# Performance work log

Measured on AMD Instinct MI355X. Metric: run time of the kernel, lower is better.

Reference implementation:

```python
import jax, jax.numpy as jnp
import numpy as np

N_HEAD = 8


def _axial_attn(x, wq, wk, wv, fw, fb, axis):
    # x: (B, T, H, W, C); axis is the axial axis in (B, nh, T, H, W, d): 2=T, 3=H, 4=W
    B, T, H, W, C = x.shape
    d = C // N_HEAD

    def heads(y):
        # (B,T,H,W,C) -> (B, nh, T, H, W, d)
        return jnp.moveaxis(y.reshape(B, T, H, W, N_HEAD, d), -2, 1)

    q, k, v = heads(x @ wq), heads(x @ wk), heads(x @ wv)
    # restrict attention to the axial axis: move it to -2, all other dims are batch
    q = jnp.moveaxis(q, axis, -2)
    k = jnp.moveaxis(k, axis, -2)
    v = jnp.moveaxis(v, axis, -2)
    scale = 1.0 / jnp.sqrt(jnp.asarray(d, x.dtype))
    scores = jnp.einsum('...ld,...md->...lm', q * scale, k)
    att = jax.nn.softmax(scores, axis=-1)
    o = jnp.einsum('...lm,...md->...ld', att, v)
    o = jnp.moveaxis(o, -2, axis)            # restore axial axis position
    o = jnp.moveaxis(o, 1, -2).reshape(B, T, H, W, C)  # merge heads
    return o @ fw + fb


def setup_inputs() -> dict:
    key = jax.random.key(0)
    ks = jax.random.split(key, 16)
    C = 512
    x = jax.random.normal(ks[0], (4, C, 16, 32, 32), jnp.float32)
    s = 0.02

    def w(k):
        return jax.random.normal(k, (C, C), jnp.float32) * s

    inp = {'x': x}
    i = 1
    for ax in ('w', 'h', 't'):
        inp[f'wq_{ax}'] = w(ks[i])
        inp[f'wk_{ax}'] = w(ks[i + 1])
        inp[f'wv_{ax}'] = w(ks[i + 2])
        inp[f'fc_{ax}'] = w(ks[i + 3])
        inp[f'fb_{ax}'] = jnp.zeros((C,), jnp.float32)
        i += 4
    return inp


def reference(x, wq_w, wk_w, wv_w, fc_w, fb_w,
              wq_h, wk_h, wv_h, fc_h, fb_h,
              wq_t, wk_t, wv_t, fc_t, fb_t):
    xt = jnp.moveaxis(x, 1, -1)  # (B, C, T, H, W) -> (B, T, H, W, C)
    out = (_axial_attn(xt, wq_w, wk_w, wv_w, fc_w, fb_w, 4)   # attend along W
           + _axial_attn(xt, wq_h, wk_h, wv_h, fc_h, fb_h, 3)  # attend along H
           + _axial_attn(xt, wq_t, wk_t, wv_t, fc_t, fb_t, 2))  # attend along T
    return jnp.moveaxis(out, -1, 1)  # back to (B, C, T, H, W)
```

## Files before the change

### kernel.cpp

```cpp
#include <hip/hip_runtime.h>
#include <stdint.h>

typedef __attribute__((ext_vector_type(8))) short bf16x8;
typedef __attribute__((ext_vector_type(4))) float f32x4;

static __device__ __forceinline__ short f2bf(float f) {
  uint32_t u = __builtin_bit_cast(uint32_t, f);
  u += 0x7fffu + ((u >> 16) & 1u);
  return (short)(u >> 16);
}

static __device__ __forceinline__ void gload_lds16(const void* g, void* l) {
  __builtin_amdgcn_global_load_lds((const __attribute__((address_space(1))) void*)g,
                                   (__attribute__((address_space(3))) void*)l, 16, 0, 0);
}

#define GFENCE asm volatile("" ::: "memory")

__global__ __launch_bounds__(256) void transpose_x_k(const float* __restrict__ x,
                                                     short* __restrict__ xb) {
  __shared__ float t[64][65];
  const int pt = blockIdx.x, ct = blockIdx.y, b = blockIdx.z;
  const int tid = threadIdx.x;
#pragma unroll
  for (int i = 0; i < 16; i++) {
    int cc = i * 4 + (tid >> 6);
    int pp = tid & 63;
    t[cc][pp] = x[(size_t)(b * 512 + ct * 64 + cc) * 16384 + pt * 64 + pp];
  }
  __syncthreads();
#pragma unroll
  for (int i = 0; i < 2; i++) {
    int seg = i * 256 + tid;
    int pw = seg >> 3, c8 = seg & 7;
    short tmp[8];
#pragma unroll
    for (int k = 0; k < 8; k++) tmp[k] = f2bf(t[c8 * 8 + k][pw]);
    *(uint4*)&xb[(size_t)(b * 16384 + pt * 64 + pw) * 512 + ct * 64 + c8 * 8] =
        *(const uint4*)tmp;
  }
}

struct WPtrs {
  const float* src[12];
  short* dst[12];
  int ld[12];
};

__global__ __launch_bounds__(256) void transpose_w_k(WPtrs P) {
  __shared__ float t[64][65];
  const int kt = blockIdx.x, nt = blockIdx.y, z = blockIdx.z;
  const float* src = P.src[z];
  short* dst = P.dst[z];
  const int ld = P.ld[z];
  const int tid = threadIdx.x;
#pragma unroll
  for (int i = 0; i < 16; i++) {
    int kk = i * 4 + (tid >> 6);
    int nn = tid & 63;
    t[kk][nn] = src[(kt * 64 + kk) * 512 + nt * 64 + nn];
  }
  __syncthreads();
#pragma unroll
  for (int i = 0; i < 2; i++) {
    int seg = i * 256 + tid;
    int nn = seg >> 3, k8 = seg & 7;
    short tmp[8];
#pragma unroll
    for (int k = 0; k < 8; k++) tmp[k] = f2bf(t[k8 * 8 + k][nn]);
    *(uint4*)&dst[(size_t)(nt * 64 + nn) * ld + kt * 64 + k8 * 8] = *(const uint4*)tmp;
  }
}

__global__ void bsum_k(const float* a, const float* b, const float* c, float* o) {
  int i = blockIdx.x * 256 + threadIdx.x;
  if (i < 512) o[i] = a[i] + b[i] + c[i];
}

#define READ_B(DST, b, kh)                                                     \
  do {                                                                         \
    _Pragma("unroll") for (int ni = 0; ni < 4; ++ni) DST[ni] =                 \
        *(const bf16x8*)(smem + ((b) * 4 + 2 + (kh)) * 16384 + boff +          \
                         ni * 1024);                                           \
  } while (0)

#define READ_A(DST, b, kh, mq)                                                 \
  do {                                                                         \
    _Pragma("unroll") for (int mi = 0; mi < 4; ++mi) DST[mi] =                 \
        *(const bf16x8*)(smem + ((b) * 4 + (kh)) * 16384 + aoff +              \
                         ((mq) * 4 + mi) * 1024);                              \
  } while (0)

#define MFMAX(mq, AF, BF)                                                      \
  do {                                                                         \
    __builtin_amdgcn_s_setprio(1);                                             \
    _Pragma("unroll") for (int mi = 0; mi < 4; ++mi)                           \
        _Pragma("unroll") for (int ni = 0; ni < 4; ++ni) acc[(mq) * 4 + mi]    \
            [ni] = __builtin_amdgcn_mfma_f32_16x16x32_bf16(                    \
                AF[mi], BF[ni], acc[(mq) * 4 + mi][ni], 0, 0, 0);              \
    __builtin_amdgcn_s_setprio(0);                                             \
    GFENCE;                                                                    \
  } while (0)

#define TILE_RA(b, b2, W1, W3, S0, S1, S2, S3, RA)                             \
  do {                                                                         \
                            \
    __builtin_amdgcn_s_barrier();                                              \
    GFENCE;                                                                    \
    READ_A(afB, b, 0, 1);                                                      \
    S0;                                                                        \
    GFENCE;                                                                    \
    MFMAX(0, afA, bfA);                                                        \
                     \
    asm volatile("s_waitcnt vmcnt(" W1 ")" ::: "memory");                      \
    __builtin_amdgcn_s_barrier();                                              \
    GFENCE;                                                                    \
    READ_B(bfB, b, 1);                                                         \
    READ_A(afA, b, 1, 0);                                                      \
    S1;                                                                        \
    GFENCE;                                                                    \
    MFMAX(1, afB, bfA);                                                        \
                            \
    __builtin_amdgcn_s_barrier();                                              \
    GFENCE;                                                                    \
    READ_A(afB, b, 1, 1);                                                      \
    S2;                                                                        \
    GFENCE;                                                                    \
    MFMAX(0, afA, bfB);                                                        \
                 \
    asm volatile("s_waitcnt vmcnt(" W3 ")" ::: "memory");                      \
    __builtin_amdgcn_s_barrier();                                              \
    GFENCE;                                                                    \
    RA;                                                                        \
    S3;                                                                        \
    GFENCE;                                                                    \
    MFMAX(1, afB, bfB);                                                        \
  } while (0)

template <int MODE>
__global__ __launch_bounds__(512, 2) void gemm256_k(const short* __restrict__ A,
                                                    int lda,
                                                    const short* __restrict__ B,
                                                    int ldb, void* __restrict__ Dp,
                                                    int K, int ldd,
                                                    const float* __restrict__ bsum,
                                                    int GN) {
  extern __shared__ char smem[];
  const int tid = threadIdx.x;
  const int lane = tid & 63, wave = tid >> 6;
  const int wr = wave >> 2, wc = wave & 3;
  const int r4 = lane & 15, kl = lane >> 4;

  int bid = blockIdx.x;
  const int cpx = gridDim.x >> 3;
  bid = (bid & 7) * cpx + (bid >> 3);
  int bm, bn;
  if constexpr (MODE == 0) {
    bn = bid % GN;
    bm = bid / GN;
  } else {
    bm = bid & 1;
    bn = bid >> 1;
  }

  const int NT = K >> 6;

  const int srow = tid >> 2;
  const int schk = (tid & 3) ^ ((tid >> 3) & 3);
  const short* gA0 = A + (size_t)(bm * 256 + srow) * lda + schk * 8;
  const short* gB0 = B + (size_t)(bn * 256 + srow) * ldb + schk * 8;

  auto stage = [&](int tt, int x) {
    const short* g = (x < 2) ? gA0 : gB0;
    const size_t rstep = (size_t)128 * ((x < 2) ? lda : ldb);
    const size_t koff = (size_t)tt * 64 + (x & 1) * 32;
    char* ldst = smem + (((tt & 1) * 4 + x) * 16384) + wave * 1024;
#pragma unroll
    for (int i = 0; i < 2; ++i)
      gload_lds16(g + i * rstep + koff, ldst + i * 8192);
  };

  const int kls = kl ^ ((r4 >> 1) & 3);
  const int aoff = wr * 8192 + r4 * 64 + kls * 16;
  const int boff = wc * 4096 + r4 * 64 + kls * 16;

  f32x4 acc[8][4];
#pragma unroll
  for (int i = 0; i < 8; ++i)
#pragma unroll
    for (int j = 0; j < 4; ++j) acc[i][j] = (f32x4){0.f, 0.f, 0.f, 0.f};
  bf16x8 afA[4], afB[4], bfA[4], bfB[4];

  stage(0, 0);
  stage(0, 2);
  stage(0, 1);
  stage(0, 3);
  stage(1, 0);
  stage(1, 2);
  asm volatile("s_waitcnt vmcnt(8)" ::: "memory");
  __builtin_amdgcn_s_barrier();
  GFENCE;
  READ_B(bfA, 0, 0);
  READ_A(afA, 0, 0, 0);
  GFENCE;

  int t = 0;
  for (; t < NT - 2; ++t) {
    const int b = t & 1, b2 = b ^ 1;
    TILE_RA(b, b2, "6", "6", stage(t + 1, 1), stage(t + 1, 3), stage(t + 2, 0),
            stage(t + 2, 2), {
              READ_B(bfA, b2, 0);
              READ_A(afA, b2, 0, 0);
            });
  }
  {
    const int b = t & 1, b2 = b ^ 1;
    TILE_RA(b, b2, "6", "4", stage(t + 1, 1), stage(t + 1, 3), (void)0, (void)0, {
      READ_B(bfA, b2, 0);
      READ_A(afA, b2, 0, 0);
    });
    ++t;
  }
  {
    const int b = t & 1, b2 = b ^ 1;
    TILE_RA(b, b2, "0", "0", (void)0, (void)0, (void)0, (void)0, (void)0);
  }

  const int m0 = wr * 128 + kl * 4;
  const int n0 = wc * 64 + r4;
  if (MODE == 0) {
    short* D = (short*)Dp;
#pragma unroll
    for (int mi = 0; mi < 8; ++mi)
#pragma unroll
      for (int ni = 0; ni < 4; ++ni)
#pragma unroll
        for (int r = 0; r < 4; ++r) {
          int row = bm * 256 + m0 + mi * 16 + r;
          int col = bn * 256 + n0 + ni * 16;
          D[(size_t)row * ldd + col] = f2bf(acc[mi][ni][r]);
        }
  } else {
    float* D = (float*)Dp + (size_t)((bn * 256) >> 14) * 8388608;
#pragma unroll
    for (int mi = 0; mi < 8; ++mi)
#pragma unroll
      for (int ni = 0; ni < 4; ++ni)
#pragma unroll
        for (int r = 0; r < 4; ++r) {
          int c = bm * 256 + m0 + mi * 16 + r;
          int n = (bn * 256 + n0 + ni * 16) & 16383;
          D[(size_t)c * 16384 + n] = acc[mi][ni][r] + bsum[c];
        }
  }
}

template <int L>
__global__ __launch_bounds__(256) void attn_mfma_k(const short* __restrict__ qkv,
                                                   short* __restrict__ o, int Adiv,
                                                   int Bmul, int Cmul, int stride,
                                                   int obase, int qbase, int qld) {
  constexpr int MT = L / 16;
  constexpr int PITCH = 40;
  __shared__ short lds[4 * (32 + 64) * PITCH];
  const int tid = threadIdx.x;
  const int lane = tid & 63, wave = tid >> 6;
  short* p_lds = lds + wave * (96 * PITCH);
  short* vt = p_lds + 32 * PITCH;

  const int wid = blockIdx.x * 4 + wave;
  const int s = wid >> 3, head = wid & 7;
  const int base = (s / Adiv) * Bmul + (s % Adiv) * Cmul;
  const int r4 = lane & 15, kl = lane >> 4;

  if constexpr (L == 16) {
    for (int i = lane; i < 96 * PITCH; i += 64) p_lds[i] = 0;
  }

  bf16x8 qf[MT][2], kf[MT][2];
#pragma unroll
  for (int mi = 0; mi < MT; ++mi)
#pragma unroll
    for (int ks = 0; ks < 2; ++ks) {
      size_t nrow = (size_t)(base + (mi * 16 + r4) * stride) * qld + qbase +
                    head * 64 + ks * 32 + kl * 8;
      qf[mi][ks] = *(const bf16x8*)&qkv[nrow];
      kf[mi][ks] = *(const bf16x8*)&qkv[nrow + 512];
    }

#pragma unroll
  for (int it = 0; it < L / 8; ++it) {
    int j = (lane >> 3) + it * 8;
    uint4 u = *(const uint4*)&qkv[(size_t)(base + j * stride) * qld + qbase + 1024 +
                                  head * 64 + (lane & 7) * 8];
    ushort e[8];
    *(uint4*)e = u;
#pragma unroll
    for (int q = 0; q < 8; ++q) vt[((lane & 7) * 8 + q) * PITCH + j] = (short)e[q];
  }

  f32x4 sacc[MT][MT];
#pragma unroll
  for (int i = 0; i < MT; ++i)
#pragma unroll
    for (int j = 0; j < MT; ++j) sacc[i][j] = (f32x4){0.f, 0.f, 0.f, 0.f};
#pragma unroll
  for (int mi = 0; mi < MT; ++mi)
#pragma unroll
    for (int ni = 0; ni < MT; ++ni)
#pragma unroll
      for (int ks = 0; ks < 2; ++ks)
        sacc[mi][ni] = __builtin_amdgcn_mfma_f32_16x16x32_bf16(
            qf[mi][ks], kf[ni][ks], sacc[mi][ni], 0, 0, 0);

#pragma unroll
  for (int mi = 0; mi < MT; ++mi) {
    float mx[4], sm[4];
#pragma unroll
    for (int r = 0; r < 4; ++r) {
      float m = sacc[mi][0][r];
      if (MT == 2) m = fmaxf(m, sacc[mi][1][r]);
#pragma unroll
      for (int d = 1; d < 16; d <<= 1) m = fmaxf(m, __shfl_xor(m, d));
      mx[r] = m;
    }
#pragma unroll
    for (int ni = 0; ni < MT; ++ni)
#pragma unroll
      for (int r = 0; r < 4; ++r)
        sacc[mi][ni][r] = __expf((sacc[mi][ni][r] - mx[r]) * 0.125f);
#pragma unroll
    for (int r = 0; r < 4; ++r) {
      float t = sacc[mi][0][r];
      if (MT == 2) t += sacc[mi][1][r];
#pragma unroll
      for (int d = 1; d < 16; d <<= 1) t += __shfl_xor(t, d);
      sm[r] = 1.0f / t;
    }
#pragma unroll
    for (int ni = 0; ni < MT; ++ni)
#pragma unroll
      for (int r = 0; r < 4; ++r)
        p_lds[(mi * 16 + kl * 4 + r) * PITCH + ni * 16 + r4] =
            f2bf(sacc[mi][ni][r] * sm[r]);
  }
  asm volatile("s_waitcnt lgkmcnt(0)" ::: "memory");

  bf16x8 paf[MT], vbf[4];
#pragma unroll
  for (int mi = 0; mi < MT; ++mi)
    paf[mi] = *(const bf16x8*)&p_lds[(mi * 16 + r4) * PITCH + kl * 8];
#pragma unroll
  for (int nd = 0; nd < 4; ++nd)
    vbf[nd] = *(const bf16x8*)&vt[(nd * 16 + r4) * PITCH + kl * 8];
  f32x4 oacc[MT][4];
#pragma unroll
  for (int i = 0; i < MT; ++i)
#pragma unroll
    for (int j = 0; j < 4; ++j) oacc[i][j] = (f32x4){0.f, 0.f, 0.f, 0.f};
#pragma unroll
  for (int mi = 0; mi < MT; ++mi)
#pragma unroll
    for (int nd = 0; nd < 4; ++nd)
      oacc[mi][nd] = __builtin_amdgcn_mfma_f32_16x16x32_bf16(paf[mi], vbf[nd],
                                                             oacc[mi][nd], 0, 0, 0);

#pragma unroll
  for (int mi = 0; mi < MT; ++mi)
#pragma unroll
    for (int r = 0; r < 4; ++r) {
      int n = base + (mi * 16 + kl * 4 + r) * stride;
      size_t ob = (size_t)n * 1536 + obase + head * 64 + r4;
#pragma unroll
      for (int nd = 0; nd < 4; ++nd) o[ob + nd * 16] = f2bf(oacc[mi][nd][r]);
    }
}

extern "C" void kernel_launch(void* const* d_in, const int* in_sizes, int n_in,
                              void* d_out, int out_size, void* d_ws, size_t ws_size,
                              hipStream_t stream) {
  const float* x = (const float*)d_in[0];
  const float* wq[3];
  const float* wk[3];
  const float* wv[3];
  const float* fc[3];
  const float* fb[3];
  for (int a = 0; a < 3; a++) {
    wq[a] = (const float*)d_in[1 + a * 5];
    wk[a] = (const float*)d_in[2 + a * 5];
    wv[a] = (const float*)d_in[3 + a * 5];
    fc[a] = (const float*)d_in[4 + a * 5];
    fb[a] = (const float*)d_in[5 + a * 5];
  }
  char* ws = (char*)d_ws;
  short* xb = (short*)(ws);
  short* wqkvt = (short*)(ws + 67108864);
  short* fctA = (short*)(ws + 71827456);
  float* bsum = (float*)(ws + 73400320);
  short* ob = (short*)(ws + 73402368);
  short* qkvA = (short*)(ws + 274728960);
  float* out = (float*)d_out;

  const bool merged = ws_size >= 878708736ull;

  (void)hipFuncSetAttribute((const void*)&gemm256_k<0>,
                            hipFuncAttributeMaxDynamicSharedMemorySize, 131072);
  (void)hipFuncSetAttribute((const void*)&gemm256_k<1>,
                            hipFuncAttributeMaxDynamicSharedMemorySize, 131072);

  WPtrs P;
  for (int a = 0; a < 3; a++) {
    P.src[a * 4 + 0] = wq[a];
    P.src[a * 4 + 1] = wk[a];
    P.src[a * 4 + 2] = wv[a];
    P.src[a * 4 + 3] = fc[a];
    P.dst[a * 4 + 0] = wqkvt + (size_t)a * 1536 * 512;
    P.dst[a * 4 + 1] = wqkvt + (size_t)a * 1536 * 512 + 512 * 512;
    P.dst[a * 4 + 2] = wqkvt + (size_t)a * 1536 * 512 + 2 * 512 * 512;
    P.dst[a * 4 + 3] = fctA + a * 512;
    P.ld[a * 4 + 0] = 512;
    P.ld[a * 4 + 1] = 512;
    P.ld[a * 4 + 2] = 512;
    P.ld[a * 4 + 3] = 1536;
  }
  transpose_w_k<<<dim3(8, 8, 12), 256, 0, stream>>>(P);
  bsum_k<<<dim3(2), 256, 0, stream>>>(fb[0], fb[1], fb[2], bsum);
  transpose_x_k<<<dim3(256, 8, 4), 256, 0, stream>>>(x, xb);

  const int Ad[3] = {1, 32, 1024};
  const int Bm_[3] = {32, 1024, 16384};
  const int Cm[3] = {0, 1, 1};
  const int St[3] = {1, 32, 1024};
  const int Ls[3] = {32, 32, 16};

  if (merged) {
    gemm256_k<0><<<dim3(4608), 512, 131072, stream>>>(
        xb, 512, wqkvt, 512, (void*)qkvA, 512, 4608, nullptr, 18);
    for (int a = 0; a < 3; a++) {
      if (Ls[a] == 32)
        attn_mfma_k<32><<<dim3(4096), 256, 0, stream>>>(
            qkvA, ob, Ad[a], Bm_[a], Cm[a], St[a], a * 512, a * 1536, 4608);
      else
        attn_mfma_k<16><<<dim3(8192), 256, 0, stream>>>(
            qkvA, ob, Ad[a], Bm_[a], Cm[a], St[a], a * 512, a * 1536, 4608);
    }
  } else {
    for (int a = 0; a < 3; a++) {
      gemm256_k<0><<<dim3(1536), 512, 131072, stream>>>(
          xb, 512, wqkvt + (size_t)a * 1536 * 512, 512, (void*)qkvA, 512, 1536,
          nullptr, 6);
      if (Ls[a] == 32)
        attn_mfma_k<32><<<dim3(4096), 256, 0, stream>>>(
            qkvA, ob, Ad[a], Bm_[a], Cm[a], St[a], a * 512, 0, 1536);
      else
        attn_mfma_k<16><<<dim3(8192), 256, 0, stream>>>(
            qkvA, ob, Ad[a], Bm_[a], Cm[a], St[a], a * 512, 0, 1536);
    }
  }
  gemm256_k<1><<<dim3(512), 512, 131072, stream>>>(
      fctA, 1536, ob, 1536, (void*)out, 1536, 0, bsum, 0);
}
```

Before: 693.9 us.

## Process two M tiles per GEMM block with continuous pipeline across tiles

Each GEMM workgroup now computes two consecutive 256-row M tiles, running the K loop over both as one software pipeline, so the prologue/drain of the second tile overlaps with the first tile's epilogue. Grids are halved accordingly. The merged single-QKV-GEMM path, used when the workspace is large enough, is removed, so the per-axis GEMM+attention sequence always runs. Halving the block count may hurt load balance, and the epilogue now sits inside the main loop, which could raise register pressure.

```diff
diff --git a/kernel.cpp b/kernel.cpp
--- a/kernel.cpp
+++ b/kernel.cpp
@@ -154,26 +154,29 @@
   int bid = blockIdx.x;
   const int cpx = gridDim.x >> 3;
   bid = (bid & 7) * cpx + (bid >> 3);
-  int bm, bn;
+  int bm0, bn;
   if constexpr (MODE == 0) {
     bn = bid % GN;
-    bm = bid / GN;
+    bm0 = (bid / GN) * 2;
   } else {
-    bm = bid & 1;
-    bn = bid >> 1;
+    bn = bid;
+    bm0 = 0;
   }
 
   const int NT = K >> 6;
+  const int V = NT * 2;
 
   const int srow = tid >> 2;
   const int schk = (tid & 3) ^ ((tid >> 3) & 3);
-  const short* gA0 = A + (size_t)(bm * 256 + srow) * lda + schk * 8;
+  const short* gA0 = A + (size_t)(bm0 * 256 + srow) * lda + schk * 8;
+  const short* gA1 = A + (size_t)((bm0 + 1) * 256 + srow) * lda + schk * 8;
   const short* gB0 = B + (size_t)(bn * 256 + srow) * ldb + schk * 8;
 
   auto stage = [&](int tt, int x) {
-    const short* g = (x < 2) ? gA0 : gB0;
+    const int tk = (tt >= NT) ? (tt - NT) : tt;
+    const short* g = (x < 2) ? ((tt >= NT) ? gA1 : gA0) : gB0;
     const size_t rstep = (size_t)128 * ((x < 2) ? lda : ldb);
-    const size_t koff = (size_t)tt * 64 + (x & 1) * 32;
+    const size_t koff = (size_t)tk * 64 + (x & 1) * 32;
     char* ldst = smem + (((tt & 1) * 4 + x) * 16384) + wave * 1024;
 #pragma unroll
     for (int i = 0; i < 2; ++i)
@@ -190,6 +193,40 @@
 #pragma unroll
     for (int j = 0; j < 4; ++j) acc[i][j] = (f32x4){0.f, 0.f, 0.f, 0.f};
   bf16x8 afA[4], afB[4], bfA[4], bfB[4];
+
+  const int m0 = wr * 128 + kl * 4;
+  const int n0 = wc * 64 + r4;
+  auto epilogue = [&](int bmx) {
+    if constexpr (MODE == 0) {
+      short* D = (short*)Dp;
+#pragma unroll
+      for (int mi = 0; mi < 8; ++mi)
+#pragma unroll
+        for (int ni = 0; ni < 4; ++ni)
+#pragma unroll
+          for (int r = 0; r < 4; ++r) {
+            int row = bmx * 256 + m0 + mi * 16 + r;
+            int col = bn * 256 + n0 + ni * 16;
+            D[(size_t)row * ldd + col] = f2bf(acc[mi][ni][r]);
+          }
+    } else {
+      float* D = (float*)Dp + (size_t)((bn * 256) >> 14) * 8388608;
+#pragma unroll
+      for (int mi = 0; mi < 8; ++mi)
+#pragma unroll
+        for (int ni = 0; ni < 4; ++ni)
+#pragma unroll
+          for (int r = 0; r < 4; ++r) {
+            int c = bmx * 256 + m0 + mi * 16 + r;
+            int n = (bn * 256 + n0 + ni * 16) & 16383;
+            D[(size_t)c * 16384 + n] = acc[mi][ni][r] + bsum[c];
+          }
+    }
+#pragma unroll
+    for (int i = 0; i < 8; ++i)
+#pragma unroll
+      for (int j = 0; j < 4; ++j) acc[i][j] = (f32x4){0.f, 0.f, 0.f, 0.f};
+  };
 
   stage(0, 0);
   stage(0, 2);
@@ -204,55 +241,29 @@
   READ_A(afA, 0, 0, 0);
   GFENCE;
 
-  int t = 0;
-  for (; t < NT - 2; ++t) {
-    const int b = t & 1, b2 = b ^ 1;
-    TILE_RA(b, b2, "6", "6", stage(t + 1, 1), stage(t + 1, 3), stage(t + 2, 0),
-            stage(t + 2, 2), {
+  int v = 0;
+  for (; v < V - 2; ++v) {
+    const int b = v & 1, b2 = b ^ 1;
+    TILE_RA(b, b2, "6", "6", stage(v + 1, 1), stage(v + 1, 3), stage(v + 2, 0),
+            stage(v + 2, 2), {
               READ_B(bfA, b2, 0);
               READ_A(afA, b2, 0, 0);
             });
+    if (v == NT - 1) epilogue(bm0);
   }
   {
-    const int b = t & 1, b2 = b ^ 1;
-    TILE_RA(b, b2, "6", "4", stage(t + 1, 1), stage(t + 1, 3), (void)0, (void)0, {
+    const int b = v & 1, b2 = b ^ 1;
+    TILE_RA(b, b2, "6", "4", stage(v + 1, 1), stage(v + 1, 3), (void)0, (void)0, {
       READ_B(bfA, b2, 0);
       READ_A(afA, b2, 0, 0);
     });
-    ++t;
+    ++v;
   }
   {
-    const int b = t & 1, b2 = b ^ 1;
+    const int b = v & 1, b2 = b ^ 1;
     TILE_RA(b, b2, "0", "0", (void)0, (void)0, (void)0, (void)0, (void)0);
   }
-
-  const int m0 = wr * 128 + kl * 4;
-  const int n0 = wc * 64 + r4;
-  if (MODE == 0) {
-    short* D = (short*)Dp;
-#pragma unroll
-    for (int mi = 0; mi < 8; ++mi)
-#pragma unroll
-      for (int ni = 0; ni < 4; ++ni)
-#pragma unroll
-        for (int r = 0; r < 4; ++r) {
-          int row = bm * 256 + m0 + mi * 16 + r;
-          int col = bn * 256 + n0 + ni * 16;
-          D[(size_t)row * ldd + col] = f2bf(acc[mi][ni][r]);
-        }
-  } else {
-    float* D = (float*)Dp + (size_t)((bn * 256) >> 14) * 8388608;
-#pragma unroll
-    for (int mi = 0; mi < 8; ++mi)
-#pragma unroll
-      for (int ni = 0; ni < 4; ++ni)
-#pragma unroll
-        for (int r = 0; r < 4; ++r) {
-          int c = bm * 256 + m0 + mi * 16 + r;
-          int n = (bn * 256 + n0 + ni * 16) & 16383;
-          D[(size_t)c * 16384 + n] = acc[mi][ni][r] + bsum[c];
-        }
-  }
+  epilogue(bm0 + 1);
 }
 
 template <int L>
@@ -401,8 +412,6 @@
   short* qkvA = (short*)(ws + 274728960);
   float* out = (float*)d_out;
 
-  const bool merged = ws_size >= 878708736ull;
-
   (void)hipFuncSetAttribute((const void*)&gemm256_k<0>,
                             hipFuncAttributeMaxDynamicSharedMemorySize, 131072);
   (void)hipFuncSetAttribute((const void*)&gemm256_k<1>,
@@ -433,30 +442,17 @@
   const int St[3] = {1, 32, 1024};
   const int Ls[3] = {32, 32, 16};
 
-  if (merged) {
-    gemm256_k<0><<<dim3(4608), 512, 131072, stream>>>(
-        xb, 512, wqkvt, 512, (void*)qkvA, 512, 4608, nullptr, 18);
-    for (int a = 0; a < 3; a++) {
-      if (Ls[a] == 32)
-        attn_mfma_k<32><<<dim3(4096), 256, 0, stream>>>(
-            qkvA, ob, Ad[a], Bm_[a], Cm[a], St[a], a * 512, a * 1536, 4608);
-      else
-        attn_mfma_k<16><<<dim3(8192), 256, 0, stream>>>(
-            qkvA, ob, Ad[a], Bm_[a], Cm[a], St[a], a * 512, a * 1536, 4608);
-    }
-  } else {
-    for (int a = 0; a < 3; a++) {
-      gemm256_k<0><<<dim3(1536), 512, 131072, stream>>>(
-          xb, 512, wqkvt + (size_t)a * 1536 * 512, 512, (void*)qkvA, 512, 1536,
-          nullptr, 6);
-      if (Ls[a] == 32)
-        attn_mfma_k<32><<<dim3(4096), 256, 0, stream>>>(
-            qkvA, ob, Ad[a], Bm_[a], Cm[a], St[a], a * 512, 0, 1536);
-      else
-        attn_mfma_k<16><<<dim3(8192), 256, 0, stream>>>(
-            qkvA, ob, Ad[a], Bm_[a], Cm[a], St[a], a * 512, 0, 1536);
-    }
-  }
-  gemm256_k<1><<<dim3(512), 512, 131072, stream>>>(
+  for (int a = 0; a < 3; a++) {
+    gemm256_k<0><<<dim3(768), 512, 131072, stream>>>(
+        xb, 512, wqkvt + (size_t)a * 1536 * 512, 512, (void*)qkvA, 512, 1536,
+        nullptr, 6);
+    if (Ls[a] == 32)
+      attn_mfma_k<32><<<dim3(4096), 256, 0, stream>>>(
+          qkvA, ob, Ad[a], Bm_[a], Cm[a], St[a], a * 512, 0, 1536);
+    else
+      attn_mfma_k<16><<<dim3(8192), 256, 0, stream>>>(
+          qkvA, ob, Ad[a], Bm_[a], Cm[a], St[a], a * 512, 0, 1536);
+  }
+  gemm256_k<1><<<dim3(256), 512, 131072, stream>>>(
       fctA, 1536, ob, 1536, (void*)out, 1536, 0, bsum, 0);
 }
```

New measurement: 881.6 us. +27.0%, slower.
